# Kernel tuning notes

Measured on AMD Instinct MI355X. Metric: run time of the kernel, lower is better.

Reference implementation:

```python
import jax, jax.numpy as jnp
import numpy as np

B, T, N, F = 16, 12, 1024, 128
H, DH, C = 8, 16, 64  # heads, d_head (=d_core//H), core_num; note d_in must equal H*DH
EPS = 1e-5


def setup_inputs() -> dict:
    key = jax.random.key(0)
    ks = jax.random.split(key, 12)
    s = lambda fan_in: 1.0 / np.sqrt(fan_in)
    return {
        "input": jax.random.normal(ks[0], (B, T, N, F), jnp.float32),
        # value Linear(d_in,d_in); weights stored [in,out]
        "W_v": jax.random.normal(ks[1], (F, F), jnp.float32) * s(F),
        "b_v": jax.random.normal(ks[2], (F,), jnp.float32) * s(F),
        # core decomposition params
        "adaptive": jax.random.normal(ks[3], (H, DH, N), jnp.float32),
        "cores": jax.random.normal(ks[4], (H, C, DH), jnp.float32),
        # FFN: Linear(2F -> 8F), GELU, Linear(8F -> F)
        "W1": jax.random.normal(ks[5], (2 * F, 8 * F), jnp.float32) * s(2 * F),
        "b1": jax.random.normal(ks[6], (8 * F,), jnp.float32) * s(2 * F),
        "W2": jax.random.normal(ks[7], (8 * F, F), jnp.float32) * s(8 * F),
        "b2": jax.random.normal(ks[8], (F,), jnp.float32) * s(8 * F),
        # BatchNorm2d(d_in) affine params (training-mode batch stats)
        "gamma": jnp.ones((F,), jnp.float32),
        "beta": jnp.zeros((F,), jnp.float32),
    }


def reference(input, W_v, b_v, adaptive, cores, W1, b1, W2, b2, gamma, beta):
    b, t, n, f = input.shape
    h, dh, _ = adaptive.shape
    # value projection, split heads: [b,t,n,f] -> [b,t,h,dh,n]
    v = input @ W_v + b_v
    v = v.reshape(b, t, n, h, dh).transpose(0, 1, 3, 4, 2)
    # core affinity scores [h,c,n]
    aff = jnp.einsum("hcd,hdn->hcn", cores, adaptive) / np.sqrt(dh)
    a_n2c = jax.nn.softmax(aff, axis=-1)  # softmax over nodes
    a_c2n = jax.nn.softmax(aff, axis=-2)  # softmax over cores
    # two-stage aggregation through cores
    v = jnp.einsum("bthfn,hcn->bthfc", v, a_n2c)
    v = jnp.einsum("bthfc,hcn->bthfn", v, a_c2n)
    # merge heads: [b,t,h,dh,n] -> [b,t,f,n] -> [b,t,n,f]
    v = v.reshape(b, t, f, n).swapaxes(-1, -2)
    # FFN on concat([input - v, v]) (dropout off in eval), residual
    x = jnp.concatenate([input - v, v], axis=-1)
    x = jax.nn.gelu(x @ W1 + b1, approximate=False) @ W2 + b2
    out = x + input
    # BatchNorm2d over channel f (batch stats over b,t,n; biased variance)
    mean = out.mean(axis=(0, 1, 2))
    var = out.var(axis=(0, 1, 2))
    return (out - mean) * jax.lax.rsqrt(var + EPS) * gamma + beta
```

## Files before the change

### kernel.cpp

```cpp
#include <hip/hip_runtime.h>
#include <math.h>

#define BB 16
#define TT 12
#define NN 1024
#define FF 128
#define BT 192
#define BTN 196608
#define CNT ((float)BTN)
#define T1SZ 1572864

typedef unsigned short ushort_t;
typedef __attribute__((ext_vector_type(8))) short bf16x8;
typedef __attribute__((ext_vector_type(4))) float f32x4;

__device__ __forceinline__ ushort_t f2bf(float x) {
    union { float f; unsigned u; } c; c.f = x;
    unsigned r = c.u + 0x7fffu + ((c.u >> 16) & 1u);
    return (ushort_t)(r >> 16);
}
__device__ __forceinline__ float bf2f(ushort_t u) {
    union { unsigned u32; float f; } c; c.u32 = ((unsigned)u) << 16; return c.f;
}
__device__ __forceinline__ unsigned pk2(float a, float b) {
    unsigned r;
    asm("v_cvt_pk_bf16_f32 %0, %1, %2" : "=v"(r) : "v"(a), "v"(b));
    return r;
}
__device__ __forceinline__ float gelu_f(float x) {
    float u = x * x;
    float s = x * fmaf(u, -0.10294428f, -2.30220852f);
    float e = __builtin_amdgcn_exp2f(s);
    return x * __builtin_amdgcn_rcpf(1.0f + e);
}

__device__ __forceinline__ char* swz256(void* base, int row, int byteoff) {
    return (char*)base + row * 256 + (byteoff ^ ((row & 7) << 4));
}

__global__ __launch_bounds__(256) void k_sm_n(const float* __restrict__ cores,
                                              const float* __restrict__ adaptive,
                                              float* __restrict__ aff,
                                              ushort_t* __restrict__ out) {
    int row = blockIdx.x;
    int h = row >> 6;
    int t = threadIdx.x;
    __shared__ float red[8];
    const float* cp = cores + row * 16;
    const float* ap = adaptive + h * 16384;
    float v0 = 0.f, v1 = 0.f, v2 = 0.f, v3 = 0.f;
#pragma unroll
    for (int d = 0; d < 16; ++d) {
        float c = cp[d];
        const float* an = ap + d * 1024;
        v0 = fmaf(c, an[t], v0);
        v1 = fmaf(c, an[t + 256], v1);
        v2 = fmaf(c, an[t + 512], v2);
        v3 = fmaf(c, an[t + 768], v3);
    }
    v0 *= 0.25f; v1 *= 0.25f; v2 *= 0.25f; v3 *= 0.25f;
    aff[row * 1024 + t]       = v0;
    aff[row * 1024 + t + 256] = v1;
    aff[row * 1024 + t + 512] = v2;
    aff[row * 1024 + t + 768] = v3;
    float m = fmaxf(fmaxf(v0, v1), fmaxf(v2, v3));
#pragma unroll
    for (int off = 32; off >= 1; off >>= 1) m = fmaxf(m, __shfl_xor(m, off));
    if ((t & 63) == 0) red[t >> 6] = m;
    __syncthreads();
    m = fmaxf(fmaxf(red[0], red[1]), fmaxf(red[2], red[3]));
    v0 = expf(v0 - m); v1 = expf(v1 - m); v2 = expf(v2 - m); v3 = expf(v3 - m);
    float s = v0 + v1 + v2 + v3;
#pragma unroll
    for (int off = 32; off >= 1; off >>= 1) s += __shfl_xor(s, off);
    __syncthreads();
    if ((t & 63) == 0) red[4 + (t >> 6)] = s;
    __syncthreads();
    s = red[4] + red[5] + red[6] + red[7];
    float inv = 1.0f / s;
    out[row * 1024 + t]       = f2bf(v0 * inv);
    out[row * 1024 + t + 256] = f2bf(v1 * inv);
    out[row * 1024 + t + 512] = f2bf(v2 * inv);
    out[row * 1024 + t + 768] = f2bf(v3 * inv);
}

__global__ __launch_bounds__(256) void k_sm_c(const float* __restrict__ aff,
                                              ushort_t* __restrict__ a_c2nT) {
    __shared__ ushort_t tile[64][72];
    int b = blockIdx.x;
    int h = b >> 4, n0 = (b & 15) * 64;
    int t = threadIdx.x;
    int nl = t >> 2, q = t & 3;
    const float* p = aff + h * 65536 + n0 + nl;
    float v[16];
    float m = -1e30f;
#pragma unroll
    for (int i = 0; i < 16; ++i) {
        v[i] = p[(q * 16 + i) * 1024];
        m = fmaxf(m, v[i]);
    }
    m = fmaxf(m, __shfl_xor(m, 1));
    m = fmaxf(m, __shfl_xor(m, 2));
    float s = 0.f;
#pragma unroll
    for (int i = 0; i < 16; ++i) { v[i] = expf(v[i] - m); s += v[i]; }
    s += __shfl_xor(s, 1);
    s += __shfl_xor(s, 2);
    float inv = 1.0f / s;
#pragma unroll
    for (int i = 0; i < 16; ++i) tile[nl][q * 16 + i] = f2bf(v[i] * inv);
    __syncthreads();
    ushort_t* ob = a_c2nT + ((size_t)h * 1024 + n0) * 64;
    for (int i = t; i < 512; i += 256) {
        int r = i >> 3, cq = i & 7;
        *(bf16x8*)&ob[r * 64 + cq * 8] = *(bf16x8*)&tile[r][cq * 8];
    }
}

__global__ __launch_bounds__(256) void k_wprep_v(const float* __restrict__ Wv,
                                                 ushort_t* __restrict__ WvT) {
    __shared__ float tile[64][65];
    int b = blockIdx.x;
    int r0 = (b >> 1) * 64, c0 = (b & 1) * 64;
    int t = threadIdx.x;
    for (int i = t; i < 4096; i += 256) {
        int r = i >> 6, c = i & 63;
        tile[r][c] = Wv[(size_t)(r0 + r) * 128 + c0 + c];
    }
    __syncthreads();
    for (int i = t; i < 4096; i += 256) {
        int c = i >> 6, r = i & 63;
        WvT[(size_t)(c0 + c) * 128 + r0 + r] = f2bf(tile[r][c]);
    }
}

__global__ __launch_bounds__(256) void k_wpack1(const float* __restrict__ W1,
                                                ushort_t* __restrict__ W1f) {
    int tid = blockIdx.x * 256 + threadIdx.x;
    int lane = tid & 63, jn = (tid >> 6) & 1, kk = (tid >> 7) & 7;
    int w = (tid >> 10) & 3, ch = tid >> 12;
    int lr = lane & 15, lg = lane >> 4;
    int n = ch * 128 + w * 32 + jn * 16 + lr;
    int kb = kk * 32 + lg * 8;
    ushort_t o[8];
#pragma unroll
    for (int e = 0; e < 8; ++e) o[e] = f2bf(W1[(size_t)(kb + e) * 1024 + n]);
    *(bf16x8*)&W1f[(size_t)tid * 8] = *(bf16x8*)o;
}

__global__ __launch_bounds__(256) void k_wpack2(const float* __restrict__ W2,
                                                ushort_t* __restrict__ W2f) {
    int tid = blockIdx.x * 256 + threadIdx.x;
    int lane = tid & 63, jy = (tid >> 6) & 1, kk = (tid >> 7) & 3;
    int w = (tid >> 9) & 3, ch = tid >> 11;
    int lr = lane & 15, lg = lane >> 4;
    int f = w * 32 + jy * 16 + lr;
    int kb = ch * 128 + kk * 32 + lg * 8;
    ushort_t o[8];
#pragma unroll
    for (int e = 0; e < 8; ++e) o[e] = f2bf(W2[(size_t)(kb + e) * 128 + f]);
    *(bf16x8*)&W2f[(size_t)tid * 8] = *(bf16x8*)o;
}

__global__ __launch_bounds__(256) void k_vs1(const float* __restrict__ input,
                                             const ushort_t* __restrict__ WvT,
                                             const float* __restrict__ bv,
                                             const ushort_t* __restrict__ a_n2c,
                                             float* __restrict__ T1p) {
    __shared__ __align__(16) ushort_t as_lds[128 * 128];
    __shared__ __align__(16) ushort_t vsT[128 * 128];
    int bt = blockIdx.x;
    int part = blockIdx.y;
    int t = threadIdx.x, w = t >> 6, lane = t & 63, lr = lane & 15, lg = lane >> 4;

    f32x4 t1acc[2][4];
#pragma unroll
    for (int hl = 0; hl < 2; ++hl)
#pragma unroll
        for (int mi = 0; mi < 4; ++mi) t1acc[hl][mi] = (f32x4){0.f, 0.f, 0.f, 0.f};

    for (int c8 = part * 2; c8 < part * 2 + 2; ++c8) {
        int n0 = c8 * 128;
        __syncthreads();
        for (int j = 0; j < 16; ++j) {
            int i = j * 256 + t;
            int r = i >> 5, cq = i & 31;
            float4 f = *(const float4*)&input[((size_t)(bt * 1024 + n0 + r)) * 128 + cq * 4];
            uint2 o;
            o.x = pk2(f.x, f.y);
            o.y = pk2(f.z, f.w);
            *(uint2*)swz256(as_lds, r, cq * 8) = o;
        }
        __syncthreads();
        f32x4 vacc[2][8];
#pragma unroll
        for (int mi = 0; mi < 2; ++mi)
#pragma unroll
            for (int jn = 0; jn < 8; ++jn) {
                float bb = bv[jn * 16 + lr];
                vacc[mi][jn] = (f32x4){bb, bb, bb, bb};
            }
#pragma unroll
        for (int ks = 0; ks < 4; ++ks) {
            bf16x8 a[2];
#pragma unroll
            for (int mi = 0; mi < 2; ++mi)
                a[mi] = *(const bf16x8*)swz256(as_lds, w * 32 + mi * 16 + lr, ks * 64 + lg * 16);
#pragma unroll
            for (int jn = 0; jn < 8; ++jn) {
                bf16x8 bfr = *(const bf16x8*)&WvT[(size_t)(jn * 16 + lr) * 128 + ks * 32 + lg * 8];
#pragma unroll
                for (int mi = 0; mi < 2; ++mi)
                    vacc[mi][jn] = __builtin_amdgcn_mfma_f32_16x16x32_bf16(a[mi], bfr, vacc[mi][jn], 0, 0, 0);
            }
        }
#pragma unroll
        for (int mi = 0; mi < 2; ++mi)
#pragma unroll
            for (int jn = 0; jn < 8; ++jn) {
                uint2 o;
                o.x = pk2(vacc[mi][jn][0], vacc[mi][jn][1]);
                o.y = pk2(vacc[mi][jn][2], vacc[mi][jn][3]);
                *(uint2*)swz256(vsT, jn * 16 + lr, w * 64 + mi * 32 + lg * 8) = o;
            }
        __syncthreads();
#pragma unroll
        for (int hl = 0; hl < 2; ++hl) {
            int h = w * 2 + hl;
#pragma unroll
            for (int ks = 0; ks < 4; ++ks) {
                bf16x8 bfr = *(const bf16x8*)swz256(vsT, h * 16 + lr, ks * 64 + lg * 16);
#pragma unroll
                for (int mi = 0; mi < 4; ++mi) {
                    bf16x8 a = *(const bf16x8*)&a_n2c[((size_t)(h * 64 + mi * 16 + lr)) * 1024 + n0 + ks * 32 + lg * 8];
                    t1acc[hl][mi] = __builtin_amdgcn_mfma_f32_16x16x32_bf16(a, bfr, t1acc[hl][mi], 0, 0, 0);
                }
            }
        }
    }
    float* op = T1p + (size_t)part * T1SZ;
#pragma unroll
    for (int hl = 0; hl < 2; ++hl) {
        int h = w * 2 + hl;
#pragma unroll
        for (int mi = 0; mi < 4; ++mi)
            *(f32x4*)&op[(((size_t)bt * 8 + h) * 16 + lr) * 64 + mi * 16 + lg * 4] = t1acc[hl][mi];
    }
}

__global__ __launch_bounds__(256) void k_t1conv(const float* __restrict__ T1p,
                                                ushort_t* __restrict__ T1t) {
    size_t i4 = ((size_t)blockIdx.x * 256 + threadIdx.x) * 4;
    float4 s = *(const float4*)&T1p[i4];
#pragma unroll
    for (int p = 1; p < 4; ++p) {
        float4 v = *(const float4*)&T1p[(size_t)p * T1SZ + i4];
        s.x += v.x; s.y += v.y; s.z += v.z; s.w += v.w;
    }
    uint2 o;
    o.x = pk2(s.x, s.y);
    o.y = pk2(s.z, s.w);
    *(uint2*)&T1t[i4] = o;
}

__global__ __launch_bounds__(256) void k_ffn(
        const float* __restrict__ input,
        const ushort_t* __restrict__ a_c2nT,
        const ushort_t* __restrict__ T1t,
        const ushort_t* __restrict__ W1f,
        const ushort_t* __restrict__ W2f,
        const float* __restrict__ b1,
        const float* __restrict__ b2,
        float* __restrict__ out,
        float* __restrict__ bn_sum,
        float* __restrict__ bn_sq) {
    __shared__ __align__(16) ushort_t x2mb[4 * 8 * 64 * 8];
    __shared__ __align__(16) ushort_t hmb[4 * 4 * 64 * 8];
    int bt = blockIdx.y;
    int n0 = blockIdx.x * 64;
    int t = threadIdx.x;
    int w = t >> 6, lane = t & 63, lr = lane & 15, lg = lane >> 4;
    int R0 = w * 16;
    int rowbase = bt * 1024 + n0;

    {
        const ushort_t* tp = T1t + ((size_t)(bt * 128) + lr) * 64 + lg * 8;
        const ushort_t* ap = a_c2nT + ((size_t)(n0 + R0 + lr)) * 64 + lg * 8;
        ushort_t* mb = x2mb + w * 4096;
        int wbase = ((lg >> 1) * 16 + lr) * 8 + (lg & 1) * 4;
#pragma unroll
        for (int h = 0; h < 8; ++h) {
            f32x4 vacc = {0.f, 0.f, 0.f, 0.f};
#pragma unroll
            for (int kk = 0; kk < 2; ++kk) {
                bf16x8 af = *(const bf16x8*)(tp + h * 1024 + kk * 32);
                bf16x8 bf = *(const bf16x8*)(ap + (size_t)h * 65536 + kk * 32);
                vacc = __builtin_amdgcn_mfma_f32_16x16x32_bf16(af, bf, vacc, 0, 0, 0);
            }
            float4 inp = *(const float4*)&input[(size_t)(rowbase + R0 + lr) * 128 + h * 16 + lg * 4];
            uint2 lft, rgt;
            lft.x = pk2(inp.x - vacc[0], inp.y - vacc[1]);
            lft.y = pk2(inp.z - vacc[2], inp.w - vacc[3]);
            rgt.x = pk2(vacc[0], vacc[1]);
            rgt.y = pk2(vacc[2], vacc[3]);
            *(uint2*)&mb[wbase + h * 256]         = lft;
            *(uint2*)&mb[wbase + (h + 8) * 256]   = rgt;
        }
    }
    __syncthreads();

    f32x4 yacc[4][2];
#pragma unroll
    for (int mi = 0; mi < 4; ++mi)
#pragma unroll
        for (int jy = 0; jy < 2; ++jy) {
            float bb = b2[w * 32 + jy * 16 + lr];
            yacc[mi][jy] = (f32x4){bb, bb, bb, bb};
        }

    int hwbase = w * 2048 + ((lg >> 1) * 16 + lr) * 8 + (lg & 1) * 4;

    for (int ch = 0; ch < 8; ++ch) {
        bf16x8 b2r[4][2];
        {
            const ushort_t* w2p = W2f + (((size_t)(ch * 4 + w) * 4) * 2) * 512 + lane * 8;
#pragma unroll
            for (int kk = 0; kk < 4; ++kk)
#pragma unroll
                for (int jy = 0; jy < 2; ++jy)
                    b2r[kk][jy] = *(const bf16x8*)(w2p + (kk * 2 + jy) * 512);
        }

        f32x4 hacc[2][4];
#pragma unroll
        for (int jn = 0; jn < 2; ++jn) {
            f32x4 bb = *(const f32x4*)&b1[ch * 128 + w * 32 + jn * 16 + lg * 4];
#pragma unroll
            for (int mi = 0; mi < 4; ++mi) hacc[jn][mi] = bb;
        }
        const ushort_t* w1p = W1f + ((size_t)(ch * 4 + w) * 16) * 512 + lane * 8;
        __builtin_amdgcn_s_setprio(1);
#pragma unroll
        for (int kk = 0; kk < 8; ++kk) {
            bf16x8 xf[4];
#pragma unroll
            for (int mi = 0; mi < 4; ++mi)
                xf[mi] = *(const bf16x8*)&x2mb[mi * 4096 + kk * 512 + lane * 8];
#pragma unroll
            for (int jn = 0; jn < 2; ++jn) {
                bf16x8 wf = *(const bf16x8*)(w1p + (kk * 2 + jn) * 512);
#pragma unroll
                for (int mi = 0; mi < 4; ++mi)
                    hacc[jn][mi] = __builtin_amdgcn_mfma_f32_16x16x32_bf16(wf, xf[mi], hacc[jn][mi], 0, 0, 0);
            }
        }
        __builtin_amdgcn_s_setprio(0);
        __syncthreads();
#pragma unroll
        for (int jn = 0; jn < 2; ++jn)
#pragma unroll
            for (int mi = 0; mi < 4; ++mi) {
                uint2 o;
                o.x = pk2(gelu_f(hacc[jn][mi][0]), gelu_f(hacc[jn][mi][1]));
                o.y = pk2(gelu_f(hacc[jn][mi][2]), gelu_f(hacc[jn][mi][3]));
                *(uint2*)&hmb[hwbase + jn * 256 + mi * 512] = o;
            }
        __syncthreads();
        __builtin_amdgcn_s_setprio(1);
#pragma unroll
        for (int kk = 0; kk < 4; ++kk) {
            bf16x8 a4[4];
#pragma unroll
            for (int mi = 0; mi < 4; ++mi)
                a4[mi] = *(const bf16x8*)&hmb[kk * 2048 + mi * 512 + lane * 8];
#pragma unroll
            for (int jy = 0; jy < 2; ++jy)
#pragma unroll
                for (int mi = 0; mi < 4; ++mi)
                    yacc[mi][jy] = __builtin_amdgcn_mfma_f32_16x16x32_bf16(a4[mi], b2r[kk][jy], yacc[mi][jy], 0, 0, 0);
        }
        __builtin_amdgcn_s_setprio(0);
    }

    float sacc[2] = {0.f, 0.f}, qacc[2] = {0.f, 0.f};
#pragma unroll
    for (int mi = 0; mi < 4; ++mi)
#pragma unroll
        for (int jy = 0; jy < 2; ++jy)
#pragma unroll
            for (int r = 0; r < 4; ++r) {
                int gr = rowbase + mi * 16 + lg * 4 + r;
                int gc = w * 32 + jy * 16 + lr;
                float val = yacc[mi][jy][r] + input[(size_t)gr * 128 + gc];
                out[(size_t)gr * 128 + gc] = val;
                sacc[jy] += val;
                qacc[jy] += val * val;
            }
#pragma unroll
    for (int jy = 0; jy < 2; ++jy) {
        float s = sacc[jy], q = qacc[jy];
        s += __shfl_xor(s, 16); s += __shfl_xor(s, 32);
        q += __shfl_xor(q, 16); q += __shfl_xor(q, 32);
        if (lg == 0) {
            atomicAdd(&bn_sum[w * 32 + jy * 16 + lr], s);
            atomicAdd(&bn_sq[w * 32 + jy * 16 + lr], q);
        }
    }
}

__global__ void k_bnfin(const float* __restrict__ bn_sum, const float* __restrict__ bn_sq,
                        const float* __restrict__ gamma, const float* __restrict__ beta,
                        float* __restrict__ scale, float* __restrict__ shift) {
    int f = threadIdx.x;
    float mean = bn_sum[f] * (1.0f / CNT);
    float var  = bn_sq[f]  * (1.0f / CNT) - mean * mean;
    float sc = gamma[f] * rsqrtf(var + 1e-5f);
    scale[f] = sc;
    shift[f] = beta[f] - mean * sc;
}

__global__ __launch_bounds__(256) void k_bnapply(float* __restrict__ out,
                                                 const float* __restrict__ scale,
                                                 const float* __restrict__ shift) {
    size_t idx = (size_t)blockIdx.x * 256 + threadIdx.x;
    int c = (int)((idx * 4) & 127);
    float4 v = *(float4*)&out[idx * 4];
    float4 sc = *(const float4*)&scale[c];
    float4 sh = *(const float4*)&shift[c];
    v.x = fmaf(v.x, sc.x, sh.x);
    v.y = fmaf(v.y, sc.y, sh.y);
    v.z = fmaf(v.z, sc.z, sh.z);
    v.w = fmaf(v.w, sc.w, sh.w);
    *(float4*)&out[idx * 4] = v;
}

extern "C" void kernel_launch(void* const* d_in, const int* in_sizes, int n_in,
                              void* d_out, int out_size, void* d_ws, size_t ws_size,
                              hipStream_t stream) {
    const float* input    = (const float*)d_in[0];
    const float* Wv       = (const float*)d_in[1];
    const float* bv       = (const float*)d_in[2];
    const float* adaptive = (const float*)d_in[3];
    const float* cores    = (const float*)d_in[4];
    const float* W1       = (const float*)d_in[5];
    const float* b1       = (const float*)d_in[6];
    const float* W2       = (const float*)d_in[7];
    const float* b2       = (const float*)d_in[8];
    const float* gamma    = (const float*)d_in[9];
    const float* beta     = (const float*)d_in[10];
    float* out = (float*)d_out;
    float* ws  = (float*)d_ws;

    float*    aff    = ws;
    ushort_t* a_n2c  = (ushort_t*)(ws + 524288);
    ushort_t* a_c2nT = (ushort_t*)(ws + 786432);
    ushort_t* T1t    = (ushort_t*)(ws + 1048576);
    ushort_t* W1f    = (ushort_t*)(ws + 1835008);
    ushort_t* W2f    = (ushort_t*)(ws + 1966080);
    ushort_t* WvT    = (ushort_t*)(ws + 2031616);
    float* bn_sum    = ws + 2039808;
    float* bn_sq     = bn_sum + 128;
    float* scale     = bn_sum + 256;
    float* shift     = bn_sum + 384;
    float* T1p       = ws + 2097152;

    k_sm_n   <<<512, 256, 0, stream>>>(cores, adaptive, aff, a_n2c);
    k_sm_c   <<<128, 256, 0, stream>>>(aff, a_c2nT);
    k_wprep_v<<<4, 256, 0, stream>>>(Wv, WvT);
    k_wpack1 <<<128, 256, 0, stream>>>(W1, W1f);
    k_wpack2 <<<64, 256, 0, stream>>>(W2, W2f);
    k_vs1    <<<dim3(BT, 4), 256, 0, stream>>>(input, WvT, bv, a_n2c, T1p);
    k_t1conv <<<1536, 256, 0, stream>>>(T1p, T1t);
    hipMemsetAsync(bn_sum, 0, 256 * sizeof(float), stream);
    k_ffn    <<<dim3(16, BT), 256, 0, stream>>>(input, a_c2nT, T1t, W1f, W2f,
                                                b1, b2, out, bn_sum, bn_sq);
    k_bnfin  <<<1, 128, 0, stream>>>(bn_sum, bn_sq, gamma, beta, scale, shift);
    k_bnapply<<<(out_size / 4) / 256, 256, 0, stream>>>(out, scale, shift);
}
```

Measured before the change: 402.3 us.

## Software-pipeline FFN chunks by overlapping next GEMM1 with current GEMM2

Restructures the FFN chunk loop so GEMM1 for the next hidden chunk runs into a second accumulator set while GEMM2 consumes the current chunk's GELU output from LDS. Two register accumulator buffers alternate across an unrolled loop. The intent is to give the scheduler independent MFMA work and hide the barrier and LDS latency between the stages. The cost is more register pressure, which may lower occupancy or cause spills.

```diff
diff --git a/kernel.cpp b/kernel.cpp
--- a/kernel.cpp
+++ b/kernel.cpp
@@ -320,67 +320,87 @@
 
     int hwbase = w * 2048 + ((lg >> 1) * 16 + lr) * 8 + (lg & 1) * 4;
 
-    for (int ch = 0; ch < 8; ++ch) {
-        bf16x8 b2r[4][2];
-        {
-            const ushort_t* w2p = W2f + (((size_t)(ch * 4 + w) * 4) * 2) * 512 + lane * 8;
-#pragma unroll
-            for (int kk = 0; kk < 4; ++kk)
-#pragma unroll
-                for (int jy = 0; jy < 2; ++jy)
-                    b2r[kk][jy] = *(const bf16x8*)(w2p + (kk * 2 + jy) * 512);
-        }
-
-        f32x4 hacc[2][4];
-#pragma unroll
-        for (int jn = 0; jn < 2; ++jn) {
-            f32x4 bb = *(const f32x4*)&b1[ch * 128 + w * 32 + jn * 16 + lg * 4];
-#pragma unroll
-            for (int mi = 0; mi < 4; ++mi) hacc[jn][mi] = bb;
-        }
-        const ushort_t* w1p = W1f + ((size_t)(ch * 4 + w) * 16) * 512 + lane * 8;
-        __builtin_amdgcn_s_setprio(1);
-#pragma unroll
-        for (int kk = 0; kk < 8; ++kk) {
-            bf16x8 xf[4];
-#pragma unroll
-            for (int mi = 0; mi < 4; ++mi)
-                xf[mi] = *(const bf16x8*)&x2mb[mi * 4096 + kk * 512 + lane * 8];
-#pragma unroll
-            for (int jn = 0; jn < 2; ++jn) {
-                bf16x8 wf = *(const bf16x8*)(w1p + (kk * 2 + jn) * 512);
-#pragma unroll
-                for (int mi = 0; mi < 4; ++mi)
-                    hacc[jn][mi] = __builtin_amdgcn_mfma_f32_16x16x32_bf16(wf, xf[mi], hacc[jn][mi], 0, 0, 0);
-            }
-        }
-        __builtin_amdgcn_s_setprio(0);
-        __syncthreads();
-#pragma unroll
-        for (int jn = 0; jn < 2; ++jn)
-#pragma unroll
-            for (int mi = 0; mi < 4; ++mi) {
-                uint2 o;
-                o.x = pk2(gelu_f(hacc[jn][mi][0]), gelu_f(hacc[jn][mi][1]));
-                o.y = pk2(gelu_f(hacc[jn][mi][2]), gelu_f(hacc[jn][mi][3]));
-                *(uint2*)&hmb[hwbase + jn * 256 + mi * 512] = o;
-            }
-        __syncthreads();
-        __builtin_amdgcn_s_setprio(1);
-#pragma unroll
-        for (int kk = 0; kk < 4; ++kk) {
-            bf16x8 a4[4];
-#pragma unroll
-            for (int mi = 0; mi < 4; ++mi)
-                a4[mi] = *(const bf16x8*)&hmb[kk * 2048 + mi * 512 + lane * 8];
-#pragma unroll
-            for (int jy = 0; jy < 2; ++jy)
-#pragma unroll
-                for (int mi = 0; mi < 4; ++mi)
-                    yacc[mi][jy] = __builtin_amdgcn_mfma_f32_16x16x32_bf16(a4[mi], b2r[kk][jy], yacc[mi][jy], 0, 0, 0);
-        }
-        __builtin_amdgcn_s_setprio(0);
-    }
+#define GEMM1_INTO(HACC, CH) {                                                        \
+        _Pragma("unroll")                                                             \
+        for (int jn = 0; jn < 2; ++jn) {                                              \
+            f32x4 bb = *(const f32x4*)&b1[(CH) * 128 + w * 32 + jn * 16 + lg * 4];    \
+            _Pragma("unroll")                                                         \
+            for (int mi = 0; mi < 4; ++mi) HACC[jn][mi] = bb;                         \
+        }                                                                             \
+        const ushort_t* w1p = W1f + ((size_t)((CH) * 4 + w) * 16) * 512 + lane * 8;   \
+        __builtin_amdgcn_s_setprio(1);                                                \
+        _Pragma("unroll")                                                             \
+        for (int kk = 0; kk < 8; ++kk) {                                              \
+            bf16x8 xf[4];                                                             \
+            _Pragma("unroll")                                                         \
+            for (int mi = 0; mi < 4; ++mi)                                            \
+                xf[mi] = *(const bf16x8*)&x2mb[mi * 4096 + kk * 512 + lane * 8];      \
+            _Pragma("unroll")                                                         \
+            for (int jn = 0; jn < 2; ++jn) {                                          \
+                bf16x8 wf = *(const bf16x8*)(w1p + (kk * 2 + jn) * 512);              \
+                _Pragma("unroll")                                                     \
+                for (int mi = 0; mi < 4; ++mi)                                        \
+                    HACC[jn][mi] = __builtin_amdgcn_mfma_f32_16x16x32_bf16(wf, xf[mi], HACC[jn][mi], 0, 0, 0); \
+            }                                                                         \
+        }                                                                             \
+        __builtin_amdgcn_s_setprio(0);                                                \
+    }
+
+#define GELU_STORE(HACC) {                                                            \
+        _Pragma("unroll")                                                             \
+        for (int jn = 0; jn < 2; ++jn)                                                \
+            _Pragma("unroll")                                                         \
+            for (int mi = 0; mi < 4; ++mi) {                                          \
+                uint2 o;                                                              \
+                o.x = pk2(gelu_f(HACC[jn][mi][0]), gelu_f(HACC[jn][mi][1]));          \
+                o.y = pk2(gelu_f(HACC[jn][mi][2]), gelu_f(HACC[jn][mi][3]));          \
+                *(uint2*)&hmb[hwbase + jn * 256 + mi * 512] = o;                      \
+            }                                                                         \
+    }
+
+#define GEMM2_CHUNK(CH) {                                                             \
+        bf16x8 b2r[4][2];                                                             \
+        const ushort_t* w2p = W2f + (((size_t)((CH) * 4 + w) * 4) * 2) * 512 + lane * 8; \
+        _Pragma("unroll")                                                             \
+        for (int kk = 0; kk < 4; ++kk)                                                \
+            _Pragma("unroll")                                                         \
+            for (int jy = 0; jy < 2; ++jy)                                            \
+                b2r[kk][jy] = *(const bf16x8*)(w2p + (kk * 2 + jy) * 512);            \
+        __builtin_amdgcn_s_setprio(1);                                                \
+        _Pragma("unroll")                                                             \
+        for (int kk = 0; kk < 4; ++kk) {                                              \
+            bf16x8 a4[4];                                                             \
+            _Pragma("unroll")                                                         \
+            for (int mi = 0; mi < 4; ++mi)                                            \
+                a4[mi] = *(const bf16x8*)&hmb[kk * 2048 + mi * 512 + lane * 8];       \
+            _Pragma("unroll")                                                         \
+            for (int jy = 0; jy < 2; ++jy)                                            \
+                _Pragma("unroll")                                                     \
+                for (int mi = 0; mi < 4; ++mi)                                        \
+                    yacc[mi][jy] = __builtin_amdgcn_mfma_f32_16x16x32_bf16(a4[mi], b2r[kk][jy], yacc[mi][jy], 0, 0, 0); \
+        }                                                                             \
+        __builtin_amdgcn_s_setprio(0);                                                \
+    }
+
+    f32x4 haccA[2][4], haccB[2][4];
+    GEMM1_INTO(haccA, 0);
+#pragma unroll
+    for (int cc = 0; cc < 4; ++cc) {
+        int ch = cc * 2;
+        __syncthreads();
+        GELU_STORE(haccA);
+        __syncthreads();
+        GEMM1_INTO(haccB, ch + 1);
+        GEMM2_CHUNK(ch);
+        __syncthreads();
+        GELU_STORE(haccB);
+        __syncthreads();
+        if (cc < 3) GEMM1_INTO(haccA, ch + 2);
+        GEMM2_CHUNK(ch + 1);
+    }
+#undef GEMM1_INTO
+#undef GELU_STORE
+#undef GEMM2_CHUNK
 
     float sacc[2] = {0.f, 0.f}, qacc[2] = {0.f, 0.f};
 #pragma unroll
```

Result: no change. 397.2 us (-1.3%).
